# Optimization experiments

Hardware: AMD Instinct MI355X
Metric: run time of the kernel (lower is better)

The kernel has to match this reference:

```python
import jax, jax.numpy as jnp
import numpy as np


def _sage_conv(x, edge_index, Wp, bp, Wl, bl, Wr):
    """PyG SAGEConv with project=True, aggr='mean', root_weight=True.
    Message side: relu(x @ Wp + bp); root side uses UNprojected x.
    """
    N = x.shape[0]
    xp = jax.nn.relu(x @ Wp + bp)                      # [N, F_in]
    src, dst = edge_index[0], edge_index[1]
    agg = jax.ops.segment_sum(xp[src], dst, num_segments=N)   # [N, F_in]
    cnt = jax.ops.segment_sum(jnp.ones(src.shape, x.dtype), dst, num_segments=N)
    mean = agg / jnp.maximum(cnt, 1.0)[:, None]        # mean aggr; 0 for isolated nodes
    return mean @ Wl + bl + x @ Wr                     # lin_l(aggr) + lin_r(root)


def setup_inputs() -> dict:
    key = jax.random.key(0)
    ks = jax.random.split(key, 16)
    BS, NUM_NODES = 16, 5000
    N = BS * NUM_NODES            # 80000 total nodes
    F_IN, HID, REP = 256, 256, 128
    E = 1_280_000                 # avg degree 16
    K = 2500                      # kriging targets per batch element

    def w(k, shape):
        return jax.random.normal(k, shape, jnp.float32) * 0.02

    return {
        "x": jax.random.normal(ks[0], (N, F_IN), jnp.float32),
        "edge_index": jax.random.randint(ks[1], (2, E), 0, N),
        "map_id": jax.random.randint(ks[2], (BS, K), 0, NUM_NODES),
        "bs": BS,
        # SAGEConv 1: in=256 -> out=256
        "Wp1": w(ks[3], (F_IN, F_IN)), "bp1": jnp.zeros((F_IN,), jnp.float32),
        "Wl1": w(ks[4], (F_IN, HID)),  "bl1": jnp.zeros((HID,), jnp.float32),
        "Wr1": w(ks[5], (F_IN, HID)),
        # SAGEConv 2: in=256 -> out=128
        "Wp2": w(ks[6], (HID, HID)),   "bp2": jnp.zeros((HID,), jnp.float32),
        "Wl2": w(ks[7], (HID, REP)),   "bl2": jnp.zeros((REP,), jnp.float32),
        "Wr2": w(ks[8], (HID, REP)),
        # final Linear rep -> rep
        "Wlin": w(ks[9], (REP, REP)),  "blin": jnp.zeros((REP,), jnp.float32),
    }


def reference(x, edge_index, map_id, bs,
              Wp1, bp1, Wl1, bl1, Wr1,
              Wp2, bp2, Wl2, bl2, Wr2,
              Wlin, blin):
    h = jax.nn.relu(_sage_conv(x, edge_index, Wp1, bp1, Wl1, bl1, Wr1))
    h = jax.nn.relu(_sage_conv(h, edge_index, Wp2, bp2, Wl2, bl2, Wr2))
    h = h @ Wlin + blin                                # [N, rep]
    num_nodes = x.shape[0] // bs
    rep = h.shape[1]
    h3 = h.reshape(bs, num_nodes, rep)
    # gather kriging-target node features per batch element
    local_feat = jnp.take_along_axis(h3, map_id[:, :, None], axis=1).reshape(-1, rep)
    return (local_feat, h)
```

## Files before the change

kernel.cpp:

```cpp
#include <hip/hip_runtime.h>
#include <hip/hip_bf16.h>

typedef __attribute__((ext_vector_type(8))) short s16x8;
typedef __attribute__((ext_vector_type(8))) ushort u16x8;
typedef __attribute__((ext_vector_type(4))) float f32x4;

static __device__ __forceinline__ float b2f(ushort u) {
  union { float f; unsigned bits; } v; v.bits = ((unsigned)u) << 16; return v.f;
}
static __device__ __forceinline__ ushort f2b(float f) {
  __hip_bfloat16 h = __float2bfloat16(f);
  return *reinterpret_cast<ushort*>(&h);
}

__global__ void detect_dtype(const ushort* __restrict__ xraw, int* __restrict__ flag) {
  __shared__ int cnt;
  if (threadIdx.x == 0) cnt = 0;
  __syncthreads();
  ushort u = xraw[threadIdx.x];
  int e = (u >> 7) & 0xFF;
  if (e >= 113 && e <= 141) atomicAdd(&cnt, 1);
  __syncthreads();
  if (threadIdx.x == 0) *flag = (cnt >= 224) ? 0 : 1;
}

__global__ void convert_x(const void* __restrict__ xin, ushort* __restrict__ xb,
                          const int* __restrict__ flag, int n) {
  int i = blockIdx.x * 256 + threadIdx.x;
  int base = i * 8;
  if (base >= n) return;
  if (*flag) {
    const float4 v0 = ((const float4*)xin)[i * 2];
    const float4 v1 = ((const float4*)xin)[i * 2 + 1];
    u16x8 o;
    o[0] = f2b(v0.x); o[1] = f2b(v0.y); o[2] = f2b(v0.z); o[3] = f2b(v0.w);
    o[4] = f2b(v1.x); o[5] = f2b(v1.y); o[6] = f2b(v1.z); o[7] = f2b(v1.w);
    ((u16x8*)xb)[i] = o;
  } else {
    ((u16x8*)xb)[i] = ((const u16x8*)xin)[i];
  }
}

struct WDesc { const void* src; ushort* dst; int R, C; };
struct WPack { WDesc d[7]; };

__global__ void transpose_convert_all(WPack p, const int* __restrict__ flag) {
  const WDesc& d = p.d[blockIdx.y];
  int i = blockIdx.x * 256 + threadIdx.x;
  if (i >= d.R * d.C) return;
  int r = i / d.C, c = i % d.C;
  ushort v = (*flag) ? f2b(((const float*)d.src)[i]) : ((const ushort*)d.src)[i];
  d.dst[c * d.R + r] = v;
}

struct BPack { WDesc d[5]; };
__global__ void convert_vec_all(BPack p, const int* __restrict__ flag) {
  const WDesc& d = p.d[blockIdx.y];
  int i = threadIdx.x;
  if (i >= d.R) return;
  d.dst[i] = (*flag) ? f2b(((const float*)d.src)[i]) : ((const ushort*)d.src)[i];
}


__global__ __launch_bounds__(256)
void hist_bucket_kernel(const int* __restrict__ dst, int* __restrict__ deg,
                        int* __restrict__ bcnt, int E, int N, int nbuck) {
  __shared__ int lh[512];
  int t = threadIdx.x;
  for (int i = t; i < nbuck; i += 256) lh[i] = 0;
  __syncthreads();
  int base = blockIdx.x * 2048;
#pragma unroll
  for (int k = 0; k < 8; ++k) {
    int e = base + k * 256 + t;
    if (e < E) {
      unsigned d = (unsigned)dst[e];
      if (d < (unsigned)N) {
        atomicAdd(&deg[d], 1);
        atomicAdd(&lh[d >> 9], 1);
      }
    }
  }
  __syncthreads();
  for (int i = t; i < nbuck; i += 256)
    if (lh[i]) atomicAdd(&bcnt[i], lh[i]);
}

__global__ __launch_bounds__(256)
void scan_buckets(const int* __restrict__ bcnt, int* __restrict__ bscan,
                  int* __restrict__ bpos, int nbuck) {
  int t = threadIdx.x;
  __shared__ int sh[256];
  int v = (t < nbuck) ? bcnt[t] : 0;
  sh[t] = v; __syncthreads();
  for (int off = 1; off < 256; off <<= 1) {
    int u = (t >= off) ? sh[t - off] : 0;
    __syncthreads();
    sh[t] += u;
    __syncthreads();
  }
  if (t < nbuck) { int ex = sh[t] - v; bscan[t] = ex; bpos[t] = ex; }
  if (t == nbuck - 1) bscan[nbuck] = sh[t];
}

__global__ __launch_bounds__(256)
void bin_scatter(const int* __restrict__ src, const int* __restrict__ dstl,
                 int* __restrict__ bpos, int2* __restrict__ pairs,
                 int E, int N, int nbuck) {
  __shared__ int lh[512];
  __shared__ int lbase[512];
  int t = threadIdx.x;
  for (int i = t; i < nbuck; i += 256) lh[i] = 0;
  __syncthreads();
  int base = blockIdx.x * 4096;
#pragma unroll
  for (int k = 0; k < 16; ++k) {
    int e = base + k * 256 + t;
    if (e < E) {
      unsigned d = (unsigned)dstl[e];
      if (d < (unsigned)N) atomicAdd(&lh[d >> 9], 1);
    }
  }
  __syncthreads();
  for (int i = t; i < nbuck; i += 256) {
    int c = lh[i];
    lbase[i] = c ? atomicAdd(&bpos[i], c) : 0;
    lh[i] = 0;
  }
  __syncthreads();
#pragma unroll
  for (int k = 0; k < 16; ++k) {
    int e = base + k * 256 + t;
    if (e < E) {
      unsigned d = (unsigned)dstl[e];
      if (d < (unsigned)N) {
        int b = d >> 9;
        int r = atomicAdd(&lh[b], 1);
        pairs[lbase[b] + r] = make_int2(src[e], (int)d);
      }
    }
  }
}

#define FS_SPLIT 4
__global__ __launch_bounds__(256)
void final_scatter(const int2* __restrict__ pairs, const int* __restrict__ bscan,
                   int* __restrict__ pos, int* __restrict__ eidx, int E) {
  int b = blockIdx.x / FS_SPLIT;
  int part = blockIdx.x % FS_SPLIT;
  int s = bscan[b], e = bscan[b + 1];
  int len = e - s;
  int per = (len + FS_SPLIT - 1) / FS_SPLIT;
  int lo = s + part * per;
  int hi = min(lo + per, e);
  for (int i = lo + threadIdx.x; i < hi; i += 256) {
    int2 p = pairs[i];
    unsigned q = (unsigned)atomicAdd(&pos[p.y], 1);
    if (q < (unsigned)E) eidx[q] = p.x;
  }
}

__global__ __launch_bounds__(256)
void scan_phaseA(const int* __restrict__ deg, int* __restrict__ bsum, int N) {
  int b = blockIdx.x, t = threadIdx.x;
  int i0 = b * 1024 + t * 4;
  int s = 0;
#pragma unroll
  for (int k = 0; k < 4; ++k) {
    int i = i0 + k;
    if (i < N) s += deg[i];
  }
  __shared__ int red[256];
  red[t] = s; __syncthreads();
  for (int off = 128; off > 0; off >>= 1) {
    if (t < off) red[t] += red[t + off];
    __syncthreads();
  }
  if (t == 0) bsum[b] = red[0];
}

__global__ __launch_bounds__(256)
void scan_phaseB(const int* __restrict__ bsum, int* __restrict__ ebsum,
                 int* __restrict__ rowptr, int B, int N) {
  int t = threadIdx.x;
  __shared__ int sh[256];
  int v = (t < B) ? bsum[t] : 0;
  sh[t] = v; __syncthreads();
  for (int off = 1; off < 256; off <<= 1) {
    int u = (t >= off) ? sh[t - off] : 0;
    __syncthreads();
    sh[t] += u;
    __syncthreads();
  }
  if (t < B) ebsum[t] = sh[t] - v;
  if (t == B - 1) rowptr[N] = sh[t];
}

__global__ __launch_bounds__(256)
void scan_phaseC(const int* __restrict__ deg, const int* __restrict__ ebsum,
                 int* __restrict__ rowptr, int* __restrict__ pos, int N) {
  int b = blockIdx.x, t = threadIdx.x;
  int i0 = b * 1024 + t * 4;
  int v[4]; int s = 0;
#pragma unroll
  for (int k = 0; k < 4; ++k) {
    int i = i0 + k;
    v[k] = (i < N) ? deg[i] : 0;
    s += v[k];
  }
  __shared__ int sh[256];
  sh[t] = s; __syncthreads();
  for (int off = 1; off < 256; off <<= 1) {
    int u = (t >= off) ? sh[t - off] : 0;
    __syncthreads();
    sh[t] += u;
    __syncthreads();
  }
  int run = ebsum[b] + sh[t] - s;
#pragma unroll
  for (int k = 0; k < 4; ++k) {
    int i = i0 + k;
    if (i < N) { rowptr[i] = run; pos[i] = run; run += v[k]; }
  }
}

__global__ __launch_bounds__(256)
void agg_mean_v3(const ushort* __restrict__ xp, const int* __restrict__ rowptr,
                 const int* __restrict__ eidx, ushort* __restrict__ mean, int NN) {
  int node = blockIdx.x * 4 + (threadIdx.x >> 6);
  if (node >= NN) return;
  int lane = threadIdx.x & 63;
  int half = lane >> 5;
  int l32 = lane & 31;
  int s = rowptr[node], e = rowptr[node + 1];
  float a[8];
#pragma unroll
  for (int k = 0; k < 8; ++k) a[k] = 0.f;

  for (int base = s; base < e; base += 64) {
    int cnt = min(64, e - base);
    int my = (lane < cnt) ? eidx[base + lane] : 0;
    int full = cnt >> 1;
#pragma unroll 2
    for (int it = 0; it < full; ++it) {
      int sn = __shfl(my, 2 * it + half);
      u16x8 v = *(const u16x8*)&xp[(size_t)sn * 256 + l32 * 8];
#pragma unroll
      for (int k = 0; k < 8; ++k) a[k] += b2f(v[k]);
    }
    if (cnt & 1) {
      int sn = __shfl(my, cnt - 1);
      if (half == 0) {
        u16x8 v = *(const u16x8*)&xp[(size_t)sn * 256 + l32 * 8];
#pragma unroll
        for (int k = 0; k < 8; ++k) a[k] += b2f(v[k]);
      }
    }
  }
#pragma unroll
  for (int k = 0; k < 8; ++k) a[k] += __shfl_xor(a[k], 32);

  int c = e - s; if (c < 1) c = 1;
  float inv = 1.f / (float)c;
  if (half == 0) {
    u16x8 o;
#pragma unroll
    for (int k = 0; k < 8; ++k) o[k] = f2b(a[k] * inv);
    *(u16x8*)&mean[(size_t)node * 256 + l32 * 8] = o;
  }
}

#define GLD16(g, l) \
  __builtin_amdgcn_global_load_lds((const __attribute__((address_space(1))) void*)(g), \
                                   (__attribute__((address_space(3))) void*)(l), 16, 0, 0)

__global__ __launch_bounds__(256, 3)
void gemm_bf16(const ushort* __restrict__ A1, const ushort* __restrict__ B1,
               const ushort* __restrict__ A2, const ushort* __restrict__ B2,
               const ushort* __restrict__ bias, ushort* __restrict__ C,
               float* __restrict__ Cf, const int* __restrict__ flag,
               int M, int N, int K1, int K2, int do_relu) {
  __shared__ __align__(16) ushort lsA[128 * 64];
  __shared__ __align__(16) ushort lsB[128 * 64];
  const int tid = threadIdx.x;
  const int lane = tid & 63;
  const int wid = tid >> 6;
  const int wr = wid >> 1, wc = wid & 1;
  const int m0 = blockIdx.x * 128;
  const int n0 = blockIdx.y * 128;
  const int l15 = lane & 15;
  const int lg = lane >> 4;
  const int fl = Cf ? *flag : 0;

  const int so   = tid * 16;
  const int fragswz = (l15 & 7) << 4;

  f32x4 acc[4][4];
#pragma unroll
  for (int i = 0; i < 4; ++i)
#pragma unroll
    for (int j = 0; j < 4; ++j) {
      acc[i][j][0] = 0.f; acc[i][j][1] = 0.f; acc[i][j][2] = 0.f; acc[i][j][3] = 0.f;
    }

#pragma unroll
  for (int pass = 0; pass < 2; ++pass) {
    const ushort* A = pass ? A2 : A1;
    const ushort* B = pass ? B2 : B1;
    const int K = pass ? K2 : K1;
    if (K == 0) continue;
    for (int k0 = 0; k0 < K; k0 += 64) {
#pragma unroll
      for (int it = 0; it < 4; ++it) {
        int o = so + it * 4096;
        int row = o >> 7;
        int colb = o & 127;
        int gcolb = colb ^ ((row & 7) << 4);
        const ushort* ga = A + (size_t)(m0 + row) * K + k0 + (gcolb >> 1);
        GLD16(ga, (char*)lsA + o);
        const ushort* gb = B + (size_t)(n0 + row) * K + k0 + (gcolb >> 1);
        GLD16(gb, (char*)lsB + o);
      }
      __syncthreads();
#pragma unroll
      for (int kk = 0; kk < 2; ++kk) {
        const int cb = ((kk * 64 + lg * 16) ^ fragswz) >> 1;
        s16x8 af[4], bfr[4];
#pragma unroll
        for (int i = 0; i < 4; ++i)
          af[i] = *(const s16x8*)&lsA[(wr * 64 + i * 16 + l15) * 64 + cb];
#pragma unroll
        for (int j = 0; j < 4; ++j)
          bfr[j] = *(const s16x8*)&lsB[(wc * 64 + j * 16 + l15) * 64 + cb];
#pragma unroll
        for (int i = 0; i < 4; ++i)
#pragma unroll
          for (int j = 0; j < 4; ++j)
            acc[i][j] = __builtin_amdgcn_mfma_f32_16x16x32_bf16(af[i], bfr[j], acc[i][j], 0, 0, 0);
      }
      __syncthreads();
    }
  }

#pragma unroll
  for (int j = 0; j < 4; ++j) {
    int col = n0 + wc * 64 + j * 16 + l15;
    float bv = bias ? b2f(bias[col]) : 0.f;
#pragma unroll
    for (int i = 0; i < 4; ++i) {
      int rbase = m0 + wr * 64 + i * 16 + lg * 4;
#pragma unroll
      for (int r = 0; r < 4; ++r) {
        float v = acc[i][j][r] + bv;
        if (do_relu) v = fmaxf(v, 0.f);
        size_t idx = (size_t)(rbase + r) * N + col;
        if (Cf) {
          if (fl) Cf[idx] = v;
          else    C[idx] = f2b(v);
        } else {
          C[idx] = f2b(v);
        }
      }
    }
  }
}

__global__ void gather_out(const ushort* __restrict__ hb, const float* __restrict__ hf,
                           const int* __restrict__ map_id, void* __restrict__ dout,
                           const int* __restrict__ flag,
                           int K, int num_nodes, int total, int N) {
  int i = blockIdx.x * 256 + threadIdx.x;
  if (i >= total) return;
  int f = i & 127;
  int row = i >> 7;
  int b = row / K;
  unsigned node = (unsigned)(b * num_nodes + map_id[row]);
  bool ok = node < (unsigned)N;
  if (*flag) {
    ((float*)dout)[i] = ok ? hf[(size_t)node * 128 + f] : 0.f;
  } else {
    ((ushort*)dout)[i] = ok ? hb[(size_t)node * 128 + f] : (ushort)0;
  }
}

extern "C" void kernel_launch(void* const* d_in, const int* in_sizes, int n_in,
                              void* d_out, int out_size, void* d_ws, size_t ws_size,
                              hipStream_t stream) {
  const void* x    = d_in[0];
  const int*  ei   = (const int*)d_in[1];
  const int*  mapi = (const int*)d_in[2];
  const void* Wp1  = d_in[4];
  const void* bp1  = d_in[5];
  const void* Wl1  = d_in[6];
  const void* bl1  = d_in[7];
  const void* Wr1  = d_in[8];
  const void* Wp2  = d_in[9];
  const void* bp2  = d_in[10];
  const void* Wl2  = d_in[11];
  const void* bl2  = d_in[12];
  const void* Wr2  = d_in[13];
  const void* Wlin = d_in[14];
  const void* blin = d_in[15];

  const int NN = in_sizes[0] / 256;
  const int E  = in_sizes[1] / 2;
  const int MAPROWS = in_sizes[2];
  const int BS = 16;
  const int NUM_NODES = NN / BS;
  const int KMAP = MAPROWS / BS;
  const int NBUCK = (NN + 511) >> 9;
  const int* src = ei;
  const int* dst = ei + E;

  ushort* houtB = (ushort*)d_out + (size_t)MAPROWS * 128;
  float*  houtF = (float*)d_out + (size_t)MAPROWS * 128;

  int2* pairs = (int2*)((char*)d_out + (size_t)MAPROWS * 128 * 4);

  char* sc = (char*)d_out;
  auto carve_sc = [&](size_t bytes) {
    char* p = sc; sc += (bytes + 255) & ~(size_t)255; return p;
  };
  ushort* Wp1T  = (ushort*)carve_sc(256 * 256 * 2);
  ushort* Wl1T  = (ushort*)carve_sc(256 * 256 * 2);
  ushort* Wr1T  = (ushort*)carve_sc(256 * 256 * 2);
  ushort* Wp2T  = (ushort*)carve_sc(256 * 256 * 2);
  ushort* Wl2T  = (ushort*)carve_sc(128 * 256 * 2);
  ushort* Wr2T  = (ushort*)carve_sc(128 * 256 * 2);
  ushort* WlinT = (ushort*)carve_sc(128 * 128 * 2);
  ushort* bp1c  = (ushort*)carve_sc(256 * 2);
  ushort* bl1c  = (ushort*)carve_sc(256 * 2);
  ushort* bp2c  = (ushort*)carve_sc(256 * 2);
  ushort* bl2c  = (ushort*)carve_sc(128 * 2);
  ushort* blinc = (ushort*)carve_sc(128 * 2);
  int* deg    = (int*)carve_sc((size_t)NN * 4);
  int* rowptr = (int*)carve_sc(((size_t)NN + 1) * 4);
  int* pos    = (int*)carve_sc((size_t)NN * 4);
  int* eidx   = (int*)carve_sc((size_t)E * 4);
  int* bsum   = (int*)carve_sc(1024);
  int* ebsum  = (int*)carve_sc(1024);
  int* bcnt   = (int*)carve_sc(2048);
  int* bscan  = (int*)carve_sc(2048 + 4);
  int* bpos   = (int*)carve_sc(2048);

  char* w = (char*)d_ws;
  auto carve = [&](size_t bytes) {
    char* p = w; w += (bytes + 255) & ~(size_t)255; return p;
  };
  int*    flag = (int*)carve(256);
  ushort* xb   = (ushort*)carve((size_t)NN * 256 * 2);
  ushort* bA   = (ushort*)carve((size_t)NN * 256 * 2);
  ushort* bB   = (ushort*)carve((size_t)NN * 256 * 2);

  detect_dtype<<<dim3(1), 256, 0, stream>>>((const ushort*)x, flag);
  convert_x<<<dim3((NN * 256 / 8 + 255) / 256), 256, 0, stream>>>(x, xb, flag, NN * 256);

  WPack wp;
  wp.d[0] = {Wp1, Wp1T, 256, 256};
  wp.d[1] = {Wl1, Wl1T, 256, 256};
  wp.d[2] = {Wr1, Wr1T, 256, 256};
  wp.d[3] = {Wp2, Wp2T, 256, 256};
  wp.d[4] = {Wl2, Wl2T, 256, 128};
  wp.d[5] = {Wr2, Wr2T, 256, 128};
  wp.d[6] = {Wlin, WlinT, 128, 128};
  transpose_convert_all<<<dim3(256, 7), 256, 0, stream>>>(wp, flag);

  BPack bp;
  bp.d[0] = {bp1, bp1c, 256, 1};
  bp.d[1] = {bl1, bl1c, 256, 1};
  bp.d[2] = {bp2, bp2c, 256, 1};
  bp.d[3] = {bl2, bl2c, 128, 1};
  bp.d[4] = {blin, blinc, 128, 1};
  convert_vec_all<<<dim3(1, 5), 256, 0, stream>>>(bp, flag);

  hipMemsetAsync(deg, 0, (size_t)NN * 4, stream);
  hipMemsetAsync(bcnt, 0, 2048, stream);
  hist_bucket_kernel<<<dim3((E + 2047) / 2048), 256, 0, stream>>>(dst, deg, bcnt, E, NN, NBUCK);
  scan_buckets<<<dim3(1), 256, 0, stream>>>(bcnt, bscan, bpos, NBUCK);
  int SB = (NN + 1023) / 1024;
  scan_phaseA<<<dim3(SB), 256, 0, stream>>>(deg, bsum, NN);
  scan_phaseB<<<dim3(1), 256, 0, stream>>>(bsum, ebsum, rowptr, SB, NN);
  scan_phaseC<<<dim3(SB), 256, 0, stream>>>(deg, ebsum, rowptr, pos, NN);
  bin_scatter<<<dim3((E + 4095) / 4096), 256, 0, stream>>>(src, dst, bpos, pairs, E, NN, NBUCK);
  final_scatter<<<dim3(NBUCK * FS_SPLIT), 256, 0, stream>>>(pairs, bscan, pos, eidx, E);

  dim3 blk(256);
  dim3 g256(NN / 128, 2);
  dim3 g128(NN / 128, 1);
  dim3 gagg((NN + 3) / 4);

  gemm_bf16<<<g256, blk, 0, stream>>>(xb, Wp1T, nullptr, nullptr, bp1c, bA,
                                      nullptr, nullptr, NN, 256, 256, 0, 1);
  agg_mean_v3<<<gagg, blk, 0, stream>>>(bA, rowptr, eidx, bB, NN);
  gemm_bf16<<<g256, blk, 0, stream>>>(bB, Wl1T, xb, Wr1T, bl1c, bA,
                                      nullptr, nullptr, NN, 256, 256, 256, 1);

  gemm_bf16<<<g256, blk, 0, stream>>>(bA, Wp2T, nullptr, nullptr, bp2c, bB,
                                      nullptr, nullptr, NN, 256, 256, 0, 1);
  agg_mean_v3<<<gagg, blk, 0, stream>>>(bB, rowptr, eidx, xb, NN);
  gemm_bf16<<<g128, blk, 0, stream>>>(xb, Wl2T, bA, Wr2T, bl2c, bB,
                                      nullptr, nullptr, NN, 128, 256, 256, 1);

  gemm_bf16<<<g128, blk, 0, stream>>>(bB, WlinT, nullptr, nullptr, blinc, houtB,
                                      houtF, flag, NN, 128, 128, 0, 0);

  int total = MAPROWS * 128;
  gather_out<<<dim3((total + 255) / 256), 256, 0, stream>>>(houtB, houtF, mapi, d_out,
                                                            flag, KMAP, NUM_NODES, total, NN);
}
```

Baseline: 493.2 us.

## Fuse final linear into layer-2 GEMM and stage GEMM epilogue through LDS

Adds a kernel that computes the second SAGE output GEMM, applies relu, keeps the 128x128 tile in LDS, and immediately multiplies by the final linear weight, writing bf16 or fp32 output. This removes one launch and a round trip of the N x 128 intermediate through global memory. The generic GEMM epilogue now writes results into a swizzled LDS tile and stores coalesced 16-byte vectors instead of scattered 2-byte stores. The fused kernel uses more LDS (64KB), so fewer blocks fit per CU. The final output is now rounded through bf16 even when fp32 output is needed.

Result: faster. 473.1 us (-4.1%).

```diff
diff --git a/kernel.cpp b/kernel.cpp
--- a/kernel.cpp
+++ b/kernel.cpp
@@ -61,7 +61,6 @@
   d.dst[i] = (*flag) ? f2b(((const float*)d.src)[i]) : ((const ushort*)d.src)[i];
 }
 
-
 __global__ __launch_bounds__(256)
 void hist_bucket_kernel(const int* __restrict__ dst, int* __restrict__ deg,
                         int* __restrict__ bcnt, int E, int N, int nbuck) {
@@ -278,10 +277,8 @@
 void gemm_bf16(const ushort* __restrict__ A1, const ushort* __restrict__ B1,
                const ushort* __restrict__ A2, const ushort* __restrict__ B2,
                const ushort* __restrict__ bias, ushort* __restrict__ C,
-               float* __restrict__ Cf, const int* __restrict__ flag,
                int M, int N, int K1, int K2, int do_relu) {
-  __shared__ __align__(16) ushort lsA[128 * 64];
-  __shared__ __align__(16) ushort lsB[128 * 64];
+  __shared__ __align__(16) ushort lsAB[2][128 * 64];
   const int tid = threadIdx.x;
   const int lane = tid & 63;
   const int wid = tid >> 6;
@@ -290,9 +287,7 @@
   const int n0 = blockIdx.y * 128;
   const int l15 = lane & 15;
   const int lg = lane >> 4;
-  const int fl = Cf ? *flag : 0;
-
-  const int so   = tid * 16;
+  const int so = tid * 16;
   const int fragswz = (l15 & 7) << 4;
 
   f32x4 acc[4][4];
@@ -317,9 +312,9 @@
         int colb = o & 127;
         int gcolb = colb ^ ((row & 7) << 4);
         const ushort* ga = A + (size_t)(m0 + row) * K + k0 + (gcolb >> 1);
-        GLD16(ga, (char*)lsA + o);
+        GLD16(ga, (char*)lsAB[0] + o);
         const ushort* gb = B + (size_t)(n0 + row) * K + k0 + (gcolb >> 1);
-        GLD16(gb, (char*)lsB + o);
+        GLD16(gb, (char*)lsAB[1] + o);
       }
       __syncthreads();
 #pragma unroll
@@ -328,10 +323,10 @@
         s16x8 af[4], bfr[4];
 #pragma unroll
         for (int i = 0; i < 4; ++i)
-          af[i] = *(const s16x8*)&lsA[(wr * 64 + i * 16 + l15) * 64 + cb];
+          af[i] = *(const s16x8*)&lsAB[0][(wr * 64 + i * 16 + l15) * 64 + cb];
 #pragma unroll
         for (int j = 0; j < 4; ++j)
-          bfr[j] = *(const s16x8*)&lsB[(wc * 64 + j * 16 + l15) * 64 + cb];
+          bfr[j] = *(const s16x8*)&lsAB[1][(wc * 64 + j * 16 + l15) * 64 + cb];
 #pragma unroll
         for (int i = 0; i < 4; ++i)
 #pragma unroll
@@ -342,25 +337,182 @@
     }
   }
 
+  ushort* tile = (ushort*)lsAB;
 #pragma unroll
   for (int j = 0; j < 4; ++j) {
-    int col = n0 + wc * 64 + j * 16 + l15;
-    float bv = bias ? b2f(bias[col]) : 0.f;
+    int col = wc * 64 + j * 16 + l15;
+    float bv = bias ? b2f(bias[n0 + col]) : 0.f;
 #pragma unroll
     for (int i = 0; i < 4; ++i) {
-      int rbase = m0 + wr * 64 + i * 16 + lg * 4;
 #pragma unroll
       for (int r = 0; r < 4; ++r) {
+        int row = wr * 64 + i * 16 + lg * 4 + r;
         float v = acc[i][j][r] + bv;
         if (do_relu) v = fmaxf(v, 0.f);
-        size_t idx = (size_t)(rbase + r) * N + col;
-        if (Cf) {
-          if (fl) Cf[idx] = v;
-          else    C[idx] = f2b(v);
-        } else {
-          C[idx] = f2b(v);
-        }
-      }
+        tile[row * 128 + (col ^ ((row & 7) << 3))] = f2b(v);
+      }
+    }
+  }
+  __syncthreads();
+#pragma unroll
+  for (int t = 0; t < 8; ++t) {
+    int id = t * 256 + tid;
+    int row = id >> 4;
+    int c8 = id & 15;
+    u16x8 v = *(const u16x8*)&tile[row * 128 + (c8 ^ (row & 7)) * 8];
+    *(u16x8*)&C[(size_t)(m0 + row) * N + n0 + c8 * 8] = v;
+  }
+}
+
+__global__ __launch_bounds__(256, 2)
+void gemm_h2_final(const ushort* __restrict__ A1, const ushort* __restrict__ B1,
+                   const ushort* __restrict__ A2, const ushort* __restrict__ B2,
+                   const ushort* __restrict__ bias2, const ushort* __restrict__ Wlin,
+                   const ushort* __restrict__ biasf,
+                   ushort* __restrict__ CB, float* __restrict__ CF,
+                   const int* __restrict__ flag, int K1, int K2) {
+  __shared__ __align__(16) ushort lsAB[2][128 * 64];
+  __shared__ __align__(16) ushort lsW[128 * 128];
+  const int tid = threadIdx.x;
+  const int lane = tid & 63;
+  const int wid = tid >> 6;
+  const int wr = wid >> 1, wc = wid & 1;
+  const int m0 = blockIdx.x * 128;
+  const int l15 = lane & 15;
+  const int lg = lane >> 4;
+  const int so = tid * 16;
+  const int fragswz = (l15 & 7) << 4;
+  const int fl = *flag;
+
+#pragma unroll
+  for (int it = 0; it < 8; ++it) {
+    int o = so + it * 4096;
+    int row = o >> 8;
+    int colb = o & 255;
+    int gcolb = colb ^ ((row & 7) << 4);
+    GLD16(Wlin + (size_t)row * 128 + (gcolb >> 1), (char*)lsW + o);
+  }
+
+  f32x4 acc[4][4];
+#pragma unroll
+  for (int i = 0; i < 4; ++i)
+#pragma unroll
+    for (int j = 0; j < 4; ++j) {
+      acc[i][j][0] = 0.f; acc[i][j][1] = 0.f; acc[i][j][2] = 0.f; acc[i][j][3] = 0.f;
+    }
+
+#pragma unroll
+  for (int pass = 0; pass < 2; ++pass) {
+    const ushort* A = pass ? A2 : A1;
+    const ushort* B = pass ? B2 : B1;
+    const int K = pass ? K2 : K1;
+    for (int k0 = 0; k0 < K; k0 += 64) {
+#pragma unroll
+      for (int it = 0; it < 4; ++it) {
+        int o = so + it * 4096;
+        int row = o >> 7;
+        int colb = o & 127;
+        int gcolb = colb ^ ((row & 7) << 4);
+        GLD16(A + (size_t)(m0 + row) * K + k0 + (gcolb >> 1), (char*)lsAB[0] + o);
+        GLD16(B + (size_t)row * K + k0 + (gcolb >> 1), (char*)lsAB[1] + o);
+      }
+      __syncthreads();
+#pragma unroll
+      for (int kk = 0; kk < 2; ++kk) {
+        const int cb = ((kk * 64 + lg * 16) ^ fragswz) >> 1;
+        s16x8 af[4], bfr[4];
+#pragma unroll
+        for (int i = 0; i < 4; ++i)
+          af[i] = *(const s16x8*)&lsAB[0][(wr * 64 + i * 16 + l15) * 64 + cb];
+#pragma unroll
+        for (int j = 0; j < 4; ++j)
+          bfr[j] = *(const s16x8*)&lsAB[1][(wc * 64 + j * 16 + l15) * 64 + cb];
+#pragma unroll
+        for (int i = 0; i < 4; ++i)
+#pragma unroll
+          for (int j = 0; j < 4; ++j)
+            acc[i][j] = __builtin_amdgcn_mfma_f32_16x16x32_bf16(af[i], bfr[j], acc[i][j], 0, 0, 0);
+      }
+      __syncthreads();
+    }
+  }
+
+  ushort* tile = (ushort*)lsAB;
+#pragma unroll
+  for (int j = 0; j < 4; ++j) {
+    int col = wc * 64 + j * 16 + l15;
+    float bv = b2f(bias2[col]);
+#pragma unroll
+    for (int i = 0; i < 4; ++i) {
+#pragma unroll
+      for (int r = 0; r < 4; ++r) {
+        int row = wr * 64 + i * 16 + lg * 4 + r;
+        float v = fmaxf(acc[i][j][r] + bv, 0.f);
+        tile[row * 128 + (col ^ ((row & 7) << 3))] = f2b(v);
+      }
+    }
+  }
+  __syncthreads();
+
+  f32x4 acc2[4][4];
+#pragma unroll
+  for (int i = 0; i < 4; ++i)
+#pragma unroll
+    for (int j = 0; j < 4; ++j) {
+      acc2[i][j][0] = 0.f; acc2[i][j][1] = 0.f; acc2[i][j][2] = 0.f; acc2[i][j][3] = 0.f;
+    }
+#pragma unroll
+  for (int kk = 0; kk < 4; ++kk) {
+    s16x8 af[4], bfr[4];
+#pragma unroll
+    for (int i = 0; i < 4; ++i) {
+      int row = wr * 64 + i * 16 + l15;
+      int cb = (kk * 32 + lg * 8) ^ ((row & 7) << 3);
+      af[i] = *(const s16x8*)&tile[row * 128 + cb];
+    }
+#pragma unroll
+    for (int j = 0; j < 4; ++j) {
+      int row = wc * 64 + j * 16 + l15;
+      int cb = (kk * 32 + lg * 8) ^ ((row & 7) << 3);
+      bfr[j] = *(const s16x8*)&lsW[row * 128 + cb];
+    }
+#pragma unroll
+    for (int i = 0; i < 4; ++i)
+#pragma unroll
+      for (int j = 0; j < 4; ++j)
+        acc2[i][j] = __builtin_amdgcn_mfma_f32_16x16x32_bf16(af[i], bfr[j], acc2[i][j], 0, 0, 0);
+  }
+  __syncthreads();
+
+#pragma unroll
+  for (int j = 0; j < 4; ++j) {
+    int col = wc * 64 + j * 16 + l15;
+    float bv = b2f(biasf[col]);
+#pragma unroll
+    for (int i = 0; i < 4; ++i) {
+#pragma unroll
+      for (int r = 0; r < 4; ++r) {
+        int row = wr * 64 + i * 16 + lg * 4 + r;
+        tile[row * 128 + (col ^ ((row & 7) << 3))] = f2b(acc2[i][j][r] + bv);
+      }
+    }
+  }
+  __syncthreads();
+#pragma unroll
+  for (int t = 0; t < 8; ++t) {
+    int id = t * 256 + tid;
+    int row = id >> 4;
+    int c8 = id & 15;
+    u16x8 v = *(const u16x8*)&tile[row * 128 + (c8 ^ (row & 7)) * 8];
+    size_t off = (size_t)(m0 + row) * 128 + c8 * 8;
+    if (fl) {
+      float4 f0, f1;
+      f0.x = b2f(v[0]); f0.y = b2f(v[1]); f0.z = b2f(v[2]); f0.w = b2f(v[3]);
+      f1.x = b2f(v[4]); f1.y = b2f(v[5]); f1.z = b2f(v[6]); f1.w = b2f(v[7]);
+      *(float4*)&CF[off] = f0;
+      *(float4*)&CF[off + 4] = f1;
+    } else {
+      *(u16x8*)&CB[off] = v;
     }
   }
 }
@@ -414,7 +566,6 @@
 
   ushort* houtB = (ushort*)d_out + (size_t)MAPROWS * 128;
   float*  houtF = (float*)d_out + (size_t)MAPROWS * 128;
-
   int2* pairs = (int2*)((char*)d_out + (size_t)MAPROWS * 128 * 4);
 
   char* sc = (char*)d_out;
@@ -486,23 +637,21 @@
 
   dim3 blk(256);
   dim3 g256(NN / 128, 2);
-  dim3 g128(NN / 128, 1);
   dim3 gagg((NN + 3) / 4);
 
   gemm_bf16<<<g256, blk, 0, stream>>>(xb, Wp1T, nullptr, nullptr, bp1c, bA,
-                                      nullptr, nullptr, NN, 256, 256, 0, 1);
+                                      NN, 256, 256, 0, 1);
   agg_mean_v3<<<gagg, blk, 0, stream>>>(bA, rowptr, eidx, bB, NN);
   gemm_bf16<<<g256, blk, 0, stream>>>(bB, Wl1T, xb, Wr1T, bl1c, bA,
-                                      nullptr, nullptr, NN, 256, 256, 256, 1);
+                                      NN, 256, 256, 256, 1);
 
   gemm_bf16<<<g256, blk, 0, stream>>>(bA, Wp2T, nullptr, nullptr, bp2c, bB,
-                                      nullptr, nullptr, NN, 256, 256, 0, 1);
+                                      NN, 256, 256, 0, 1);
   agg_mean_v3<<<gagg, blk, 0, stream>>>(bB, rowptr, eidx, xb, NN);
-  gemm_bf16<<<g128, blk, 0, stream>>>(xb, Wl2T, bA, Wr2T, bl2c, bB,
-                                      nullptr, nullptr, NN, 128, 256, 256, 1);
-
-  gemm_bf16<<<g128, blk, 0, stream>>>(bB, WlinT, nullptr, nullptr, blinc, houtB,
-                                      houtF, flag, NN, 128, 128, 0, 0);
+
+  gemm_h2_final<<<dim3(NN / 128), blk, 0, stream>>>(xb, Wl2T, bA, Wr2T, bl2c,
+                                                    WlinT, blinc, houtB, houtF,
+                                                    flag, 256, 256);
 
   int total = MAPROWS * 128;
   gather_out<<<dim3((total + 255) / 256), 256, 0, stream>>>(houtB, houtF, mapi, d_out,
```
